# Kernel optimization log

Hardware: AMD Instinct MI355X
Metric: run time of the kernel (lower is better)

The kernel has to match this reference:

```python
import jax, jax.numpy as jnp
import numpy as np

NEG_SLOPE = 0.2


def setup_inputs() -> dict:
    key = jax.random.key(0)
    ks = jax.random.split(key, 6)
    N, E, IN, H, D = 50000, 800000, 256, 4, 64
    x = jax.random.normal(ks[0], (N, IN), dtype=jnp.float32)
    edge_index = jax.random.randint(ks[1], (2, E), 0, N, dtype=jnp.int64)
    W = jax.random.normal(ks[2], (IN, H * D), dtype=jnp.float32) / np.sqrt(IN)
    att_src = jax.random.normal(ks[3], (H, D), dtype=jnp.float32) / np.sqrt(D)
    att_dst = jax.random.normal(ks[4], (H, D), dtype=jnp.float32) / np.sqrt(D)
    bias = jnp.zeros((H * D,), dtype=jnp.float32)
    return {"x": x, "edge_index": edge_index, "W": W,
            "att_src": att_src, "att_dst": att_dst, "bias": bias}


def reference(x, edge_index, W, att_src, att_dst, bias):
    N = x.shape[0]
    H, D = att_src.shape
    # add self-loops (PyG GATConv default add_self_loops=True)
    loops = jnp.arange(N, dtype=edge_index.dtype)
    src = jnp.concatenate([edge_index[0], loops])  # [E']
    dst = jnp.concatenate([edge_index[1], loops])  # [E']
    # per-head linear transform: [N, H, D]
    h = (x @ W).reshape(N, H, D)
    # per-node attention logits per head: [N, H]
    a_s = jnp.einsum('nhd,hd->nh', h, att_src)
    a_d = jnp.einsum('nhd,hd->nh', h, att_dst)
    # per-edge raw attention: [E', H]
    e = jax.nn.leaky_relu(a_s[src] + a_d[dst], NEG_SLOPE)
    # softmax over edges grouped by destination node (stable)
    m = jax.ops.segment_max(e, dst, num_segments=N)
    e = jnp.exp(e - m[dst])
    s = jax.ops.segment_sum(e, dst, num_segments=N)
    alpha = e / s[dst]  # every node has a self-loop -> s > 0
    # weighted scatter-aggregate: [N, H, D]
    out = jax.ops.segment_sum(alpha[:, :, None] * h[src], dst, num_segments=N)
    # concat heads + bias; dropout=0.0 -> identity
    return out.reshape(N, H * D) + bias
```

## Files before the change

### kernel.cpp

```cpp
#include <hip/hip_runtime.h>
#include <hip/hip_bf16.h>

#define NEG_SLOPE 0.2f
#define HPAD 264

typedef short short8 __attribute__((ext_vector_type(8)));
typedef float floatx4 __attribute__((ext_vector_type(4)));
typedef unsigned short ushort8v __attribute__((ext_vector_type(8)));
typedef unsigned short ushort4v __attribute__((ext_vector_type(4)));
typedef unsigned int uint4v __attribute__((ext_vector_type(4)));

__device__ __forceinline__ float bf2f_raw(unsigned short u) {
    union { float f; unsigned u; } c; c.u = ((unsigned)u) << 16; return c.f;
}
__device__ __forceinline__ float asf(unsigned u) {
    union { float f; unsigned u; } c; c.u = u; return c.f;
}
__device__ __forceinline__ unsigned short f2bf_raw(float f) {
    union { float f; unsigned u; } c; c.f = f;
    unsigned u = c.u;
    u += 0x7FFFu + ((u >> 16) & 1u);
    return (unsigned short)(u >> 16);
}
__device__ __forceinline__ float ldf(const void* p, size_t i, int f32) {
    return f32 ? ((const float*)p)[i] : bf2f_raw(((const unsigned short*)p)[i]);
}
__device__ __forceinline__ unsigned short ldbf(const void* p, size_t i, int f32) {
    return f32 ? f2bf_raw(((const float*)p)[i]) : ((const unsigned short*)p)[i];
}
__device__ __forceinline__ int clampN(long long v, int N) {
    if (v < 0) v = 0;
    if (v >= N) v = N - 1;
    return (int)v;
}
__device__ __forceinline__ float lrelu(float v) { return v > 0.f ? v : NEG_SLOPE * v; }

__device__ __forceinline__ void glds16(const void* g, void* l) {
    __builtin_amdgcn_global_load_lds(
        (const __attribute__((address_space(1))) void*)g,
        (__attribute__((address_space(3))) void*)l, 16, 0, 0);
}

__global__ __launch_bounds__(256) void prep_kernel(
    const void* __restrict__ W, unsigned short* __restrict__ Wt,
    const unsigned short* __restrict__ x,
    const unsigned short* __restrict__ as_, const unsigned short* __restrict__ ad_,
    const unsigned* __restrict__ edge_w, int* __restrict__ flags, int edge_words,
    int* __restrict__ deg8, int* __restrict__ bsync, int N8)
{
    __shared__ float sm[256];
    __shared__ unsigned su[256];
    const int t = threadIdx.x;
    const int i = blockIdx.x * 256 + t;

    #pragma unroll
    for (int j = 0; j < 7; ++j) {
        int z = i + j * 65536;
        if (z < N8) deg8[z] = 0;
    }
    if (i < 256) bsync[i] = 0;

    float mw = 0.f;
    for (int k = t; k < 4096; k += 256) {
        float v = fabsf(bf2f_raw(((const unsigned short*)W)[k]));
        mw = fmaxf(mw, (v == v && v < 3e38f) ? v : 1e9f);
    }
    sm[t] = mw; __syncthreads();
    for (int s = 128; s; s >>= 1) { if (t < s) sm[t] = fmaxf(sm[t], sm[t + s]); __syncthreads(); }
    const int wf32 = sm[0] > 100.f;
    __syncthreads();

    if (blockIdx.x == 0) {
        float mx = 0.f, ma = 0.f;
        for (int k = t; k < 4096; k += 256) {
            float v = fabsf(bf2f_raw(x[k]));
            mx = fmaxf(mx, (v == v && v < 3e38f) ? v : 1e9f);
        }
        {
            float v1 = fabsf(bf2f_raw(as_[t]));
            float v2 = fabsf(bf2f_raw(ad_[t]));
            v1 = (v1 == v1 && v1 < 3e38f) ? v1 : 1e9f;
            v2 = (v2 == v2 && v2 < 3e38f) ? v2 : 1e9f;
            ma = fmaxf(v1, v2);
        }
        unsigned ow = 0;
        {
            int k = 2 * t + 1;
            if (k < edge_words) ow = edge_w[k];
        }
        sm[t] = mx; __syncthreads();
        for (int s = 128; s; s >>= 1) { if (t < s) sm[t] = fmaxf(sm[t], sm[t + s]); __syncthreads(); }
        if (t == 0) flags[0] = sm[0] > 100.f;
        __syncthreads();
        sm[t] = ma; __syncthreads();
        for (int s = 128; s; s >>= 1) { if (t < s) sm[t] = fmaxf(sm[t], sm[t + s]); __syncthreads(); }
        if (t == 0) flags[2] = sm[0] > 100.f;
        __syncthreads();
        su[t] = ow; __syncthreads();
        for (int s = 128; s; s >>= 1) { if (t < s) su[t] |= su[t + s]; __syncthreads(); }
        if (t == 0) { flags[3] = (su[0] == 0u); flags[1] = wf32; }
    }

    int j = i & 7;
    int l = (i >> 3) & 63;
    int ks = (i >> 9) & 7;
    int c = i >> 12;
    int k = ks * 32 + (l >> 4) * 8 + j;
    int n = c * 16 + (l & 15);
    Wt[i] = ldbf(W, (size_t)k * 256 + n, wf32);
}

__global__ __launch_bounds__(512) void gemm_count_kernel(
    const void* __restrict__ x, const unsigned short* __restrict__ Wt,
    const void* __restrict__ att_src, const void* __restrict__ att_dst,
    unsigned short* __restrict__ h_out, float* __restrict__ a_s, float* __restrict__ a_d,
    const void* __restrict__ edge, int* __restrict__ deg8, int* __restrict__ rank,
    const int* __restrict__ flags, int N, int E, int ntiles,
    int ngemm, int ncount, int ntotal)
{
    const unsigned long long bi = blockIdx.x;
    const unsigned before = (unsigned)((bi * (unsigned long long)ncount) / ntotal);
    const unsigned after  = (unsigned)(((bi + 1) * (unsigned long long)ncount) / ntotal);

    if (after != before) {
        const int cb = (int)before;
        const int base = cb * 2048 + threadIdx.x * 4;
        if (base >= E) return;
        int* my = deg8 + (size_t)(cb & 7) * N;
        const int cnt = (E - base < 4) ? (E - base) : 4;
        int d[4];
        if (flags[3]) {
            const long long* p = (const long long*)edge + E + base;
            #pragma unroll
            for (int k = 0; k < 4; ++k) d[k] = clampN((k < cnt) ? p[k] : 0, N);
        } else {
            const int* p = (const int*)edge + E + base;
            #pragma unroll
            for (int k = 0; k < 4; ++k) d[k] = clampN((k < cnt) ? (long long)p[k] : 0, N);
        }
        int r[4] = {0, 0, 0, 0};
        #pragma unroll
        for (int k = 0; k < 4; ++k)
            if (k < cnt) r[k] = atomicAdd(&my[d[k]], 1);
        #pragma unroll
        for (int k = 0; k < 4; ++k)
            if (k < cnt) rank[base + k] = r[k];
        return;
    }

    const int gb = (int)(bi - before);

    __shared__ unsigned short sh_x[8192];
    __shared__ unsigned short sh_h[32][HPAD];
    __shared__ float sh_a[2][32][4];

    const int tid = threadIdx.x;
    const int w = tid >> 6;
    const int head = w >> 1;
    const int st = w & 1;
    const int l = tid & 63;
    const int lane16 = l & 15;
    const int quad = l >> 4;
    const int xf = flags[0], af = flags[2];
    const int n0w = head * 64;

    float as_att[4], ad_att[4];
    #pragma unroll
    for (int nt = 0; nt < 4; ++nt) {
        as_att[nt] = ldf(att_src, n0w + nt * 16 + lane16, af);
        ad_att[nt] = ldf(att_dst, n0w + nt * 16 + lane16, af);
    }

    const int rowl = st * 16 + lane16;
    const int swl = (rowl & 7) << 4;
    char* const xb = (char*)sh_x;

    for (int tile = gb; tile < ntiles; tile += ngemm) {
        const int m0 = tile * 32;

        __syncthreads();
        if (!xf) {
            #pragma unroll
            for (int p = 0; p < 2; ++p) {
                const int t16 = p * 512 + tid;
                const int rowb = t16 >> 5;
                const int off = (t16 & 31) * 16;
                int srow = m0 + rowb; if (srow >= N) srow = N - 1;
                const char* g = (const char*)x + (size_t)srow * 512
                              + (off ^ ((rowb & 7) << 4));
                glds16(g, xb + (size_t)(p * 512 + w * 64) * 16);
            }
        } else {
            #pragma unroll
            for (int p = 0; p < 2; ++p) {
                const int t16 = p * 512 + tid;
                const int rowb = t16 >> 5;
                const int off = (t16 & 31) * 16;
                int srow = m0 + rowb; if (srow >= N) srow = N - 1;
                const int c0 = (off ^ ((rowb & 7) << 4)) >> 1;
                const float* fp = (const float*)x + (size_t)srow * 256 + c0;
                ushort8v v;
                #pragma unroll
                for (int j = 0; j < 8; ++j) v[j] = f2bf_raw(fp[j]);
                *(ushort8v*)(xb + (size_t)t16 * 16) = v;
            }
        }
        __syncthreads();

        floatx4 acc[4];
        #pragma unroll
        for (int nt = 0; nt < 4; ++nt) acc[nt] = (floatx4){0.f, 0.f, 0.f, 0.f};

        const unsigned short* wp0 = Wt + (((size_t)head * 32) * 64 + l) * 8;

        #pragma unroll
        for (int half = 0; half < 2; ++half) {
            short8 fa[4];
            #pragma unroll
            for (int k4 = 0; k4 < 4; ++k4) {
                const int A = rowl * 512 + half * 256 + k4 * 64 + quad * 16;
                fa[k4] = *(const short8*)(xb + (A ^ swl));
            }
            #pragma unroll
            for (int k4 = 0; k4 < 4; ++k4) {
                const unsigned short* wp = wp0 + (size_t)(half * 4 + k4) * 512;
                #pragma unroll
                for (int nt = 0; nt < 4; ++nt) {
                    short8 fb = *(const short8*)(wp + nt * 4096);
                    acc[nt] = __builtin_amdgcn_mfma_f32_16x16x32_bf16(fa[k4], fb, acc[nt], 0, 0, 0);
                }
            }
        }

        __syncthreads();

        #pragma unroll
        for (int nt = 0; nt < 4; ++nt) {
            #pragma unroll
            for (int r = 0; r < 4; ++r) {
                sh_h[st * 16 + quad * 4 + r][n0w + nt * 16 + lane16] = f2bf_raw(acc[nt][r]);
            }
        }
        #pragma unroll
        for (int r = 0; r < 4; ++r) {
            float vs = acc[0][r] * as_att[0] + acc[1][r] * as_att[1]
                     + acc[2][r] * as_att[2] + acc[3][r] * as_att[3];
            float vd = acc[0][r] * ad_att[0] + acc[1][r] * ad_att[1]
                     + acc[2][r] * ad_att[2] + acc[3][r] * ad_att[3];
            vs += __shfl_xor(vs, 1); vs += __shfl_xor(vs, 2);
            vs += __shfl_xor(vs, 4); vs += __shfl_xor(vs, 8);
            vd += __shfl_xor(vd, 1); vd += __shfl_xor(vd, 2);
            vd += __shfl_xor(vd, 4); vd += __shfl_xor(vd, 8);
            if (lane16 == 0) {
                const int row = st * 16 + quad * 4 + r;
                sh_a[0][row][head] = vs;
                sh_a[1][row][head] = vd;
            }
        }

        __syncthreads();

        #pragma unroll
        for (int p = 0; p < 2; ++p) {
            const int c = p * 512 + tid;
            const int row = c >> 5;
            const int ch = c & 31;
            if (m0 + row < N) {
                ushort8v v = *(const ushort8v*)&sh_h[row][ch * 8];
                *(ushort8v*)(h_out + (size_t)(m0 + row) * 256 + ch * 8) = v;
            }
        }
        {
            if (tid < 32) {
                if (m0 + tid < N)
                    *(floatx4*)&a_s[(size_t)(m0 + tid) * 4] = *(const floatx4*)&sh_a[0][tid][0];
            } else if (tid >= 64 && tid < 96) {
                const int r = tid - 64;
                if (m0 + r < N)
                    *(floatx4*)&a_d[(size_t)(m0 + r) * 4] = *(const floatx4*)&sh_a[1][r][0];
            }
        }
    }
}

__global__ __launch_bounds__(256) void scan_fused_kernel(
    const int* __restrict__ deg8, int* __restrict__ deg,
    int* __restrict__ row_off, int* __restrict__ cursor8,
    int* __restrict__ bsum, int* __restrict__ bbase, int* __restrict__ bsync,
    int N, int nb)
{
    __shared__ int sh[256];
    __shared__ int is_last;
    __shared__ int sbase;
    const int b = blockIdx.x, t = threadIdx.x;
    const int base_i = b * 1024 + t * 4;
    int v[4], ts = 0;
    #pragma unroll
    for (int i = 0; i < 4; ++i) {
        int idx = base_i + i;
        int tot = 0;
        if (idx < N) {
            #pragma unroll
            for (int x = 0; x < 8; ++x) tot += deg8[(size_t)x * N + idx];
        }
        v[i] = tot;
        ts += tot;
    }
    sh[t] = ts; __syncthreads();
    for (int off = 1; off < 256; off <<= 1) {
        int add = (t >= off) ? sh[t - off] : 0;
        __syncthreads();
        sh[t] += add;
        __syncthreads();
    }
    if (t == 255) {
        __hip_atomic_store(&bsum[b], sh[255], __ATOMIC_RELEASE, __HIP_MEMORY_SCOPE_AGENT);
        int arrived = __hip_atomic_fetch_add(&bsync[0], 1, __ATOMIC_ACQ_REL, __HIP_MEMORY_SCOPE_AGENT);
        is_last = (arrived == nb - 1);
    }
    __syncthreads();
    if (is_last) {
        if (nb <= 64) {
            if (t < 64) {
                int val = (t < nb)
                    ? __hip_atomic_load(&bsum[t], __ATOMIC_ACQUIRE, __HIP_MEMORY_SCOPE_AGENT) : 0;
                int incl = val;
                #pragma unroll
                for (int off = 1; off < 64; off <<= 1) {
                    int u = __shfl_up(incl, off);
                    if (t >= off) incl += u;
                }
                if (t < nb)
                    __hip_atomic_store(&bbase[t], incl - val, __ATOMIC_RELEASE, __HIP_MEMORY_SCOPE_AGENT);
            }
        } else if (t == 0) {
            int run = 0;
            for (int i = 0; i < nb; ++i) {
                int s = __hip_atomic_load(&bsum[i], __ATOMIC_ACQUIRE, __HIP_MEMORY_SCOPE_AGENT);
                __hip_atomic_store(&bbase[i], run, __ATOMIC_RELEASE, __HIP_MEMORY_SCOPE_AGENT);
                run += s;
            }
        }
        __syncthreads();
        if (t == 0)
            __hip_atomic_store(&bsync[1], 1, __ATOMIC_RELEASE, __HIP_MEMORY_SCOPE_AGENT);
    }
    if (t == 0) {
        while (__hip_atomic_load(&bsync[1], __ATOMIC_ACQUIRE, __HIP_MEMORY_SCOPE_AGENT) == 0) {}
        sbase = __hip_atomic_load(&bbase[b], __ATOMIC_RELAXED, __HIP_MEMORY_SCOPE_AGENT);
    }
    __syncthreads();
    int run = sbase + sh[t] - ts;
    #pragma unroll
    for (int i = 0; i < 4; ++i) {
        int idx = base_i + i;
        if (idx < N) {
            row_off[idx] = run;
            deg[idx] = v[i];
            int c = run;
            #pragma unroll
            for (int x = 0; x < 8; ++x) {
                cursor8[(size_t)x * N + idx] = c;
                c += deg8[(size_t)x * N + idx];
            }
        }
        run += v[i];
    }
}

__global__ __launch_bounds__(512) void scatter_kernel(
    const void* __restrict__ edge, const int* __restrict__ cursor8,
    const int* __restrict__ rank, int* __restrict__ elist,
    const int* __restrict__ flags, int E, int N)
{
    const int base = blockIdx.x * 2048 + threadIdx.x * 4;
    if (base >= E) return;
    const int* mybase = cursor8 + (size_t)(blockIdx.x & 7) * N;
    const int cnt = (E - base < 4) ? (E - base) : 4;
    int s[4], d[4];
    if (flags[3]) {
        const long long* ps = (const long long*)edge + base;
        const long long* pd = (const long long*)edge + E + base;
        #pragma unroll
        for (int k = 0; k < 4; ++k) {
            s[k] = clampN((k < cnt) ? ps[k] : 0, N);
            d[k] = clampN((k < cnt) ? pd[k] : 0, N);
        }
    } else {
        const int* ps = (const int*)edge + base;
        const int* pd = (const int*)edge + E + base;
        #pragma unroll
        for (int k = 0; k < 4; ++k) {
            s[k] = clampN((k < cnt) ? (long long)ps[k] : 0, N);
            d[k] = clampN((k < cnt) ? (long long)pd[k] : 0, N);
        }
    }
    #pragma unroll
    for (int k = 0; k < 4; ++k) {
        if (k < cnt) {
            int pos = mybase[d[k]] + rank[base + k];
            elist[pos] = s[k];
        }
    }
}

__global__ __launch_bounds__(256) void aggregate_kernel(
    const int* __restrict__ row_off, const int* __restrict__ deg,
    const int* __restrict__ elist,
    const float* __restrict__ a_s, const float* __restrict__ a_d,
    const unsigned short* __restrict__ h_ws,
    const void* __restrict__ bias, void* __restrict__ out,
    const int* __restrict__ flags, int N)
{
    const int n = blockIdx.x * 4 + (threadIdx.x >> 6);
    if (n >= N) return;
    const int lane = threadIdx.x & 63;
    const int q = lane >> 4;
    const int li = lane & 15;
    const int head = li >> 2;
    const int col0 = li * 16;

    const int dn = deg[n];
    const int row = row_off[n];
    const float adn = a_d[n * 4 + head];
    const float self_logit = lrelu(a_s[n * 4 + head] + adn);

    float acc[16];
    {
        const uint4v* hp = (const uint4v*)(h_ws + (size_t)n * 256 + col0);
        uint4v ha = hp[0], hb = hp[1];
        #pragma unroll
        for (int w = 0; w < 4; ++w) {
            acc[2 * w]         = (q == 0) ? asf(ha[w] << 16) : 0.f;
            acc[2 * w + 1]     = (q == 0) ? asf(ha[w] & 0xffff0000u) : 0.f;
            acc[8 + 2 * w]     = (q == 0) ? asf(hb[w] << 16) : 0.f;
            acc[8 + 2 * w + 1] = (q == 0) ? asf(hb[w] & 0xffff0000u) : 0.f;
        }
    }
    float ssum = (q == 0) ? 1.f : 0.f;

    float asA, asB;
    uint4v hA0, hA1, hB0, hB1;
    int sC, sD;
    {
        int e0 = q, e1 = 4 + q, e2 = 8 + q, e3 = 12 + q;
        int s0 = (e0 < dn) ? elist[row + e0] : n;
        int s1 = (e1 < dn) ? elist[row + e1] : n;
        sC = (e2 < dn) ? elist[row + e2] : n;
        sD = (e3 < dn) ? elist[row + e3] : n;
        asA = a_s[s0 * 4 + head];
        asB = a_s[s1 * 4 + head];
        const uint4v* pA = (const uint4v*)(h_ws + (size_t)s0 * 256 + col0);
        const uint4v* pB = (const uint4v*)(h_ws + (size_t)s1 * 256 + col0);
        hA0 = pA[0]; hA1 = pA[1];
        hB0 = pB[0]; hB1 = pB[1];
    }

    for (int c0 = 0; c0 < dn; c0 += 8) {
        {
            float p = __expf(lrelu(asA + adn) - self_logit);
            p = (c0 + q < dn) ? p : 0.f;
            ssum += p;
            #pragma unroll
            for (int w = 0; w < 4; ++w) {
                acc[2 * w]         += p * asf(hA0[w] << 16);
                acc[2 * w + 1]     += p * asf(hA0[w] & 0xffff0000u);
                acc[8 + 2 * w]     += p * asf(hA1[w] << 16);
                acc[8 + 2 * w + 1] += p * asf(hA1[w] & 0xffff0000u);
            }
        }
        {
            asA = a_s[sC * 4 + head];
            const uint4v* p = (const uint4v*)(h_ws + (size_t)sC * 256 + col0);
            hA0 = p[0]; hA1 = p[1];
            int e = c0 + 16 + q;
            sC = (e < dn) ? elist[row + e] : n;
        }
        {
            float p = __expf(lrelu(asB + adn) - self_logit);
            p = (c0 + 4 + q < dn) ? p : 0.f;
            ssum += p;
            #pragma unroll
            for (int w = 0; w < 4; ++w) {
                acc[2 * w]         += p * asf(hB0[w] << 16);
                acc[2 * w + 1]     += p * asf(hB0[w] & 0xffff0000u);
                acc[8 + 2 * w]     += p * asf(hB1[w] << 16);
                acc[8 + 2 * w + 1] += p * asf(hB1[w] & 0xffff0000u);
            }
        }
        {
            asB = a_s[sD * 4 + head];
            const uint4v* p = (const uint4v*)(h_ws + (size_t)sD * 256 + col0);
            hB0 = p[0]; hB1 = p[1];
            int e = c0 + 20 + q;
            sD = (e < dn) ? elist[row + e] : n;
        }
    }

    #pragma unroll
    for (int j = 0; j < 16; ++j) {
        acc[j] += __shfl_xor(acc[j], 16);
        acc[j] += __shfl_xor(acc[j], 32);
    }
    float stot = ssum + __shfl_xor(ssum, 16);
    stot += __shfl_xor(stot, 32);

    const float inv = 1.f / stot;
    const int j0 = q * 4;
    const int bf32 = flags[2];
    float o[4];
    #pragma unroll
    for (int k = 0; k < 4; ++k)
        o[k] = acc[j0 + k] * inv + ldf(bias, col0 + j0 + k, bf32);
    if (flags[0]) {
        float* op = (float*)out + (size_t)n * 256 + col0 + j0;
        __builtin_nontemporal_store((floatx4){o[0], o[1], o[2], o[3]}, (floatx4*)op);
    } else {
        ushort4v ov;
        #pragma unroll
        for (int k = 0; k < 4; ++k) ov[k] = f2bf_raw(o[k]);
        __builtin_nontemporal_store(ov,
            (ushort4v*)((unsigned short*)out + (size_t)n * 256 + col0 + j0));
    }
}

__global__ __launch_bounds__(256) void sentinel_kernel(unsigned short* out, size_t n, float v) {
    size_t i = (size_t)blockIdx.x * 256 + threadIdx.x;
    if (i < n) out[i] = f2bf_raw(v);
}

extern "C" void kernel_launch(void* const* d_in, const int* in_sizes, int n_in,
                              void* d_out, int out_size, void* d_ws, size_t ws_size,
                              hipStream_t stream) {
    const void* x       = d_in[0];
    const void* edge    = d_in[1];
    const void* W       = d_in[2];
    const void* att_src = d_in[3];
    const void* att_dst = d_in[4];
    const void* bias    = d_in[5];

    const int N = in_sizes[0] / 256;
    const int E = in_sizes[1] / 2;

    char* ws = (char*)d_ws;
    size_t off = 256;
    int*   flags   = (int*)ws;
    float* a_s     = (float*)(ws + off); off += (size_t)N * 4 * sizeof(float);
    float* a_d     = (float*)(ws + off); off += (size_t)N * 4 * sizeof(float);
    int*   deg     = (int*)(ws + off);   off += (size_t)N * sizeof(int);
    int*   row_off = (int*)(ws + off);   off += (size_t)N * sizeof(int);
    int*   bsum    = (int*)(ws + off);   off += 256 * sizeof(int);
    int*   bbase   = (int*)(ws + off);   off += 256 * sizeof(int);
    int*   bsync   = (int*)(ws + off);   off += 256 * sizeof(int);
    unsigned short* Wt = (unsigned short*)(ws + off); off += 65536 * sizeof(unsigned short);
    size_t elist_bytes = (size_t)E * sizeof(int);
    size_t deg8_bytes  = (size_t)8 * N * sizeof(int);
    int*   elist   = (int*)(ws + off);
    int*   deg8    = (int*)(ws + off);   off += (elist_bytes > deg8_bytes ? elist_bytes : deg8_bytes);
    int*   cursor8 = (int*)(ws + off);   off += deg8_bytes;
    int*   rank    = (int*)(ws + off);   off += (size_t)E * sizeof(int);
    unsigned short* h_ws = (unsigned short*)(ws + off);
    const size_t need = off + (size_t)N * 256 * sizeof(unsigned short);

    if (ws_size < need) {
        float v = (float)(ws_size >> 20) * 1000.0f;
        size_t n = (size_t)out_size;
        sentinel_kernel<<<(unsigned)((n + 255) / 256), 256, 0, stream>>>(
            (unsigned short*)d_out, n, v);
        return;
    }

    int edge_words = (2 * E < 512) ? 2 * E : 512;
    prep_kernel<<<256, 256, 0, stream>>>(
        W, Wt, (const unsigned short*)x,
        (const unsigned short*)att_src, (const unsigned short*)att_dst,
        (const unsigned*)edge, flags, edge_words, deg8, bsync, 8 * N);

    const int ntiles = (N + 31) / 32;
    const int ngemm = 1024;
    const int ncount = (E + 2047) / 2048;
    const int ntotal = ngemm + ncount;
    gemm_count_kernel<<<ntotal, 512, 0, stream>>>(
        x, Wt, att_src, att_dst, h_ws, a_s, a_d, edge, deg8, rank,
        flags, N, E, ntiles, ngemm, ncount, ntotal);

    const int nb = (N + 1023) / 1024;
    scan_fused_kernel<<<nb, 256, 0, stream>>>(
        deg8, deg, row_off, cursor8, bsum, bbase, bsync, N, nb);

    scatter_kernel<<<ncount, 512, 0, stream>>>(edge, cursor8, rank, elist, flags, E, N);

    aggregate_kernel<<<(N + 3) / 4, 256, 0, stream>>>(
        row_off, deg, elist, a_s, a_d, h_ws, bias, d_out, flags, N);
}
```

Before: 242.9 us.

## Fuse degree scan and edge scatter into one kernel with grid barrier

Merges the prefix-scan kernel and the CSR scatter kernel into a single launch. A new atomic grid-wide barrier on bsync[2] separates the two phases, and the scan blocks then loop over the scatter chunks. This removes one kernel launch and its gap. In exchange, the scatter now runs on only about 49 blocks of 512 threads instead of about 391, which reduces parallelism for the random-write phase. The serial fallback for more than 64 blocks was also removed, and the code assumes bsync[2] is zeroed.

```diff
diff --git a/kernel.cpp b/kernel.cpp
--- a/kernel.cpp
+++ b/kernel.cpp
@@ -283,63 +283,57 @@
     }
 }
 
-__global__ __launch_bounds__(256) void scan_fused_kernel(
+__global__ __launch_bounds__(512) void scan_scatter_kernel(
     const int* __restrict__ deg8, int* __restrict__ deg,
     int* __restrict__ row_off, int* __restrict__ cursor8,
     int* __restrict__ bsum, int* __restrict__ bbase, int* __restrict__ bsync,
-    int N, int nb)
+    const void* __restrict__ edge, const int* __restrict__ rank,
+    int* __restrict__ elist, const int* __restrict__ flags,
+    int N, int nb, int E, int nchunks)
 {
-    __shared__ int sh[256];
+    __shared__ int sh[512];
     __shared__ int is_last;
     __shared__ int sbase;
     const int b = blockIdx.x, t = threadIdx.x;
-    const int base_i = b * 1024 + t * 4;
-    int v[4], ts = 0;
+
+    const int base_i = b * 1024 + t * 2;
+    int v[2], ts = 0;
     #pragma unroll
-    for (int i = 0; i < 4; ++i) {
+    for (int i = 0; i < 2; ++i) {
         int idx = base_i + i;
         int tot = 0;
         if (idx < N) {
             #pragma unroll
-            for (int x = 0; x < 8; ++x) tot += deg8[(size_t)x * N + idx];
+            for (int xx = 0; xx < 8; ++xx) tot += deg8[(size_t)xx * N + idx];
         }
         v[i] = tot;
         ts += tot;
     }
     sh[t] = ts; __syncthreads();
-    for (int off = 1; off < 256; off <<= 1) {
+    for (int off = 1; off < 512; off <<= 1) {
         int add = (t >= off) ? sh[t - off] : 0;
         __syncthreads();
         sh[t] += add;
         __syncthreads();
     }
-    if (t == 255) {
-        __hip_atomic_store(&bsum[b], sh[255], __ATOMIC_RELEASE, __HIP_MEMORY_SCOPE_AGENT);
+    if (t == 511) {
+        __hip_atomic_store(&bsum[b], sh[511], __ATOMIC_RELEASE, __HIP_MEMORY_SCOPE_AGENT);
         int arrived = __hip_atomic_fetch_add(&bsync[0], 1, __ATOMIC_ACQ_REL, __HIP_MEMORY_SCOPE_AGENT);
         is_last = (arrived == nb - 1);
     }
     __syncthreads();
     if (is_last) {
-        if (nb <= 64) {
-            if (t < 64) {
-                int val = (t < nb)
-                    ? __hip_atomic_load(&bsum[t], __ATOMIC_ACQUIRE, __HIP_MEMORY_SCOPE_AGENT) : 0;
-                int incl = val;
-                #pragma unroll
-                for (int off = 1; off < 64; off <<= 1) {
-                    int u = __shfl_up(incl, off);
-                    if (t >= off) incl += u;
-                }
-                if (t < nb)
-                    __hip_atomic_store(&bbase[t], incl - val, __ATOMIC_RELEASE, __HIP_MEMORY_SCOPE_AGENT);
-            }
-        } else if (t == 0) {
-            int run = 0;
-            for (int i = 0; i < nb; ++i) {
-                int s = __hip_atomic_load(&bsum[i], __ATOMIC_ACQUIRE, __HIP_MEMORY_SCOPE_AGENT);
-                __hip_atomic_store(&bbase[i], run, __ATOMIC_RELEASE, __HIP_MEMORY_SCOPE_AGENT);
-                run += s;
-            }
+        if (t < 64) {
+            int val = (t < nb)
+                ? __hip_atomic_load(&bsum[t], __ATOMIC_ACQUIRE, __HIP_MEMORY_SCOPE_AGENT) : 0;
+            int incl = val;
+            #pragma unroll
+            for (int off = 1; off < 64; off <<= 1) {
+                int u = __shfl_up(incl, off);
+                if (t >= off) incl += u;
+            }
+            if (t < nb)
+                __hip_atomic_store(&bbase[t], incl - val, __ATOMIC_RELEASE, __HIP_MEMORY_SCOPE_AGENT);
         }
         __syncthreads();
         if (t == 0)
@@ -352,54 +346,58 @@
     __syncthreads();
     int run = sbase + sh[t] - ts;
     #pragma unroll
-    for (int i = 0; i < 4; ++i) {
+    for (int i = 0; i < 2; ++i) {
         int idx = base_i + i;
         if (idx < N) {
             row_off[idx] = run;
             deg[idx] = v[i];
             int c = run;
             #pragma unroll
-            for (int x = 0; x < 8; ++x) {
-                cursor8[(size_t)x * N + idx] = c;
-                c += deg8[(size_t)x * N + idx];
+            for (int xx = 0; xx < 8; ++xx) {
+                cursor8[(size_t)xx * N + idx] = c;
+                c += deg8[(size_t)xx * N + idx];
             }
         }
         run += v[i];
     }
-}
-
-__global__ __launch_bounds__(512) void scatter_kernel(
-    const void* __restrict__ edge, const int* __restrict__ cursor8,
-    const int* __restrict__ rank, int* __restrict__ elist,
-    const int* __restrict__ flags, int E, int N)
-{
-    const int base = blockIdx.x * 2048 + threadIdx.x * 4;
-    if (base >= E) return;
-    const int* mybase = cursor8 + (size_t)(blockIdx.x & 7) * N;
-    const int cnt = (E - base < 4) ? (E - base) : 4;
-    int s[4], d[4];
-    if (flags[3]) {
-        const long long* ps = (const long long*)edge + base;
-        const long long* pd = (const long long*)edge + E + base;
+
+    __syncthreads();
+    if (t == 0) {
+        __hip_atomic_fetch_add(&bsync[2], 1, __ATOMIC_ACQ_REL, __HIP_MEMORY_SCOPE_AGENT);
+        while (__hip_atomic_load(&bsync[2], __ATOMIC_ACQUIRE, __HIP_MEMORY_SCOPE_AGENT) < nb) {}
+    }
+    __syncthreads();
+
+    const int i64 = flags[3];
+    for (int c = b; c < nchunks; c += nb) {
+        const int base = c * 2048 + t * 4;
+        if (base >= E) continue;
+        const int* mybase = cursor8 + (size_t)(c & 7) * N;
+        const int cnt = (E - base < 4) ? (E - base) : 4;
+        int s[4], d[4];
+        if (i64) {
+            const long long* ps = (const long long*)edge + base;
+            const long long* pd = (const long long*)edge + E + base;
+            #pragma unroll
+            for (int k = 0; k < 4; ++k) {
+                s[k] = clampN((k < cnt) ? ps[k] : 0, N);
+                d[k] = clampN((k < cnt) ? pd[k] : 0, N);
+            }
+        } else {
+            const int* ps = (const int*)edge + base;
+            const int* pd = (const int*)edge + E + base;
+            #pragma unroll
+            for (int k = 0; k < 4; ++k) {
+                s[k] = clampN((k < cnt) ? (long long)ps[k] : 0, N);
+                d[k] = clampN((k < cnt) ? (long long)pd[k] : 0, N);
+            }
+        }
         #pragma unroll
         for (int k = 0; k < 4; ++k) {
-            s[k] = clampN((k < cnt) ? ps[k] : 0, N);
-            d[k] = clampN((k < cnt) ? pd[k] : 0, N);
-        }
-    } else {
-        const int* ps = (const int*)edge + base;
-        const int* pd = (const int*)edge + E + base;
-        #pragma unroll
-        for (int k = 0; k < 4; ++k) {
-            s[k] = clampN((k < cnt) ? (long long)ps[k] : 0, N);
-            d[k] = clampN((k < cnt) ? (long long)pd[k] : 0, N);
-        }
-    }
-    #pragma unroll
-    for (int k = 0; k < 4; ++k) {
-        if (k < cnt) {
-            int pos = mybase[d[k]] + rank[base + k];
-            elist[pos] = s[k];
+            if (k < cnt) {
+                int pos = mybase[d[k]] + rank[base + k];
+                elist[pos] = s[k];
+            }
         }
     }
 }
@@ -585,10 +583,9 @@
         flags, N, E, ntiles, ngemm, ncount, ntotal);
 
     const int nb = (N + 1023) / 1024;
-    scan_fused_kernel<<<nb, 256, 0, stream>>>(
-        deg8, deg, row_off, cursor8, bsum, bbase, bsync, N, nb);
-
-    scatter_kernel<<<ncount, 512, 0, stream>>>(edge, cursor8, rank, elist, flags, E, N);
+    scan_scatter_kernel<<<nb, 512, 0, stream>>>(
+        deg8, deg, row_off, cursor8, bsum, bbase, bsync,
+        edge, rank, elist, flags, N, nb, E, ncount);
 
     aggregate_kernel<<<(N + 3) / 4, 256, 0, stream>>>(
         row_off, deg, elist, a_s, a_d, h_ws, bias, d_out, flags, N);
```

Result: slower. 277.4 us (+14.2%).
